# Optimization experiments

Measured on AMD Instinct MI355X. Metric: run time of the kernel, lower is better.

The kernel has to match this reference:

```python
import jax, jax.numpy as jnp
import numpy as np

N = 400000   # active voxels (submanifold: N' == N)
K3 = 27      # kernel_size**3
D = 64       # in_channels
DP = 64      # out_channels


def setup_inputs() -> dict:
    key = jax.random.key(0)
    k1, k2, k3 = jax.random.split(key, 3)
    feats = jax.random.normal(k1, (N, D), dtype=jnp.float32)
    # neighbor index table: indices[k, n] = row of feats contributing at kernel
    # offset k for output site n; negative would mean 'no neighbor' (masked).
    indices = jax.random.randint(k2, (K3, N), 0, N, dtype=jnp.int64)
    weight = jax.random.normal(k3, (K3, D, DP), dtype=jnp.float32)
    return {"feats": feats, "indices": indices, "weight": weight}


def reference(feats, indices, weight):
    # Submanifold sparse conv as implicit GEMM:
    #   out[n] = sum_k feats[indices[k, n]] @ weight[k]   (skip indices < 0)
    # Scan over the K^3 kernel offsets (fixed, small) to avoid materializing
    # the full [K3, N, D] gathered tensor.
    n_out = indices.shape[1]
    dp = weight.shape[2]

    def body(acc, kw):
        idx, w = kw                                   # idx: [N'], w: [D, DP]
        valid = (idx >= 0)[:, None]                   # [N', 1]
        g = jnp.where(valid, feats[jnp.maximum(idx, 0)], 0.0)  # [N', D]
        return acc + g @ w, None

    init = jnp.zeros((n_out, dp), dtype=feats.dtype)
    out, _ = jax.lax.scan(body, init, (indices, weight))
    return out
```

## Files before the change

kernel.cpp:

```cpp
#include <hip/hip_runtime.h>
#include <hip/hip_bf16.h>
#include <stdint.h>

typedef __bf16 bf16_t;
typedef bf16_t bf16x8 __attribute__((ext_vector_type(8)));
typedef float f32x4 __attribute__((ext_vector_type(4)));

#define D_IN 64
#define D_OUT 64
#define BM 256
#define NTHREADS 512

#define GLOAD_LDS16(gsrc, ldst)                                                     \
    __builtin_amdgcn_global_load_lds(                                               \
        (const __attribute__((address_space(1))) uint32_t*)(gsrc),                  \
        (__attribute__((address_space(3))) uint32_t*)(ldst), 16, 0, 0)

__device__ __forceinline__ uint32_t swz(int row, int col) {
    return (uint32_t)((row * 128 + col * 2) ^ ((row & 7) << 4));
}

__global__ void convert_feats(const float* __restrict__ feats,
                              bf16_t* __restrict__ fb,
                              int n_elems, int total8) {
    int g = blockIdx.x * blockDim.x + threadIdx.x;
    for (; g < total8; g += gridDim.x * blockDim.x) {
        const int e = g * 8;
        bf16x8 v = {};
        if (e < n_elems) {
            f32x4 a = *(const f32x4*)(feats + e);
            f32x4 b = *(const f32x4*)(feats + e + 4);
            #pragma unroll
            for (int i = 0; i < 4; ++i) {
                v[i]     = (bf16_t)a[i];
                v[i + 4] = (bf16_t)b[i];
            }
        }
        *(bf16x8*)(fb + e) = v;
    }
}

__global__ void convert_weight(const float* __restrict__ w,
                               bf16_t* __restrict__ wtb, int k3) {
    const int k = blockIdx.x;
    const int tid = threadIdx.x;
    const int dp = tid >> 3;
    const int cp = tid & 7;
    const int d0 = (cp ^ (dp & 7)) * 8;
    const float* src = w + (size_t)k * (D_IN * D_OUT) + (size_t)d0 * D_OUT + dp;
    bf16x8 v;
    #pragma unroll
    for (int j = 0; j < 8; ++j) v[j] = (bf16_t)src[j * D_OUT];
    *(bf16x8*)((char*)wtb + (size_t)k * 8192 + tid * 16) = v;
}

__global__ __launch_bounds__(NTHREADS, 4) void subm_conv_256(
    const bf16_t* __restrict__ fb,
    const int* __restrict__ indices,
    const bf16_t* __restrict__ wtb,
    float* __restrict__ out,
    int n_vox, int k3)
{
    __shared__ __align__(16) bf16_t As[2][BM * 64];
    __shared__ __align__(16) bf16_t Bs[2][64 * 64];

    const int tid  = threadIdx.x;
    const int lane = tid & 63;
    const int wv   = tid >> 6;
    const int l15  = lane & 15;
    const int l4   = lane >> 4;
    const int wr   = (wv >> 1) * 64;
    const int wc   = (wv & 1) * 32;
    const int n0   = blockIdx.x * BM;

    const int rbase = wv * 32 + (lane >> 3);
    const uint32_t so = (uint32_t)(((lane & 7) ^ ((lane >> 3) & 7)) * 16);

    int ia0, ia1, ia2, ia3;

    #define LOADIDX(kk) do {                                                   \
        const int* ip = indices + (size_t)(kk) * n_vox + n0 + rbase;           \
        ia0 = (n0 + rbase      < n_vox) ? ip[0]  : -1;                         \
        ia1 = (n0 + rbase + 8  < n_vox) ? ip[8]  : -1;                         \
        ia2 = (n0 + rbase + 16 < n_vox) ? ip[16] : -1;                         \
        ia3 = (n0 + rbase + 24 < n_vox) ? ip[24] : -1;                         \
    } while (0)

    #define STAGE(buf, kk) do {                                                \
        GLOAD_LDS16((const char*)wtb + (size_t)(kk) * 8192 + tid * 16,         \
                    (char*)&Bs[buf][0] + wv * 1024);                           \
        const size_t r0_ = (size_t)((ia0 >= 0 && ia0 < n_vox) ? ia0 : n_vox);  \
        const size_t r1_ = (size_t)((ia1 >= 0 && ia1 < n_vox) ? ia1 : n_vox);  \
        const size_t r2_ = (size_t)((ia2 >= 0 && ia2 < n_vox) ? ia2 : n_vox);  \
        const size_t r3_ = (size_t)((ia3 >= 0 && ia3 < n_vox) ? ia3 : n_vox);  \
        char* ad_ = (char*)&As[buf][0] + wv * 4096;                            \
        GLOAD_LDS16((const char*)fb + r0_ * 128 + so, ad_);                    \
        GLOAD_LDS16((const char*)fb + r1_ * 128 + so, ad_ + 1024);             \
        GLOAD_LDS16((const char*)fb + r2_ * 128 + so, ad_ + 2048);             \
        GLOAD_LDS16((const char*)fb + r3_ * 128 + so, ad_ + 3072);             \
    } while (0)

    f32x4 acc[4][2];
    #pragma unroll
    for (int i = 0; i < 4; ++i)
        #pragma unroll
        for (int j = 0; j < 2; ++j)
            acc[i][j] = (f32x4){0.f, 0.f, 0.f, 0.f};

    LOADIDX(0);
    STAGE(0, 0);
    if (k3 > 1) LOADIDX(1);

    for (int k = 0; k < k3; ++k) {
        __syncthreads();

        if (k + 1 < k3) STAGE((k + 1) & 1, k + 1);
        if (k + 2 < k3) LOADIDX(k + 2);

        const char* ab = (const char*)&As[k & 1][0];
        const char* bb = (const char*)&Bs[k & 1][0];
        #pragma unroll
        for (int ks = 0; ks < 2; ++ks) {
            const int kc = ks * 32 + l4 * 8;
            bf16x8 b0 = *(const bf16x8*)(bb + swz(wc + l15,      kc));
            bf16x8 b1 = *(const bf16x8*)(bb + swz(wc + 16 + l15, kc));
            #pragma unroll
            for (int mi = 0; mi < 4; ++mi) {
                bf16x8 a = *(const bf16x8*)(ab + swz(wr + mi * 16 + l15, kc));
                acc[mi][0] = __builtin_amdgcn_mfma_f32_16x16x32_bf16(a, b0, acc[mi][0], 0, 0, 0);
                acc[mi][1] = __builtin_amdgcn_mfma_f32_16x16x32_bf16(a, b1, acc[mi][1], 0, 0, 0);
            }
        }
    }

    #pragma unroll
    for (int mi = 0; mi < 4; ++mi)
        #pragma unroll
        for (int ni = 0; ni < 2; ++ni)
            #pragma unroll
            for (int j = 0; j < 4; ++j) {
                const int row = n0 + wr + mi * 16 + l4 * 4 + j;
                const int col = wc + ni * 16 + l15;
                if (row < n_vox)
                    out[(size_t)row * D_OUT + col] = acc[mi][ni][j];
            }
    #undef LOADIDX
    #undef STAGE
}

__global__ __launch_bounds__(512, 1) void subm_conv_mfma_v1(
    const float* __restrict__ feats,
    const int* __restrict__ indices,
    const float* __restrict__ weight,
    float* __restrict__ out,
    int n_vox, int k3)
{
    __shared__ bf16_t As[128 * 64];
    __shared__ bf16_t Bs[64 * 64];

    const int tid  = threadIdx.x;
    const int lane = tid & 63;
    const int wv   = tid >> 6;
    const int wr   = (wv >> 1) * 32;
    const int wc   = (wv & 1) * 32;
    const int l15  = lane & 15;
    const int l4   = lane >> 4;
    const int n0   = blockIdx.x * 128;

    const int ar = tid >> 2;
    const int ac = (tid & 3) * 16;
    const int bdp = tid & 63;
    const int bd0 = (tid >> 6) * 8;

    f32x4 acc[2][2];
    #pragma unroll
    for (int i = 0; i < 2; ++i)
        #pragma unroll
        for (int j = 0; j < 2; ++j)
            acc[i][j] = (f32x4){0.f, 0.f, 0.f, 0.f};

    for (int k = 0; k < k3; ++k) {
        __syncthreads();
        {
            const int n = n0 + ar;
            int idx = (n < n_vox) ? indices[(size_t)k * n_vox + n] : -1;
            bf16x8 v0 = {}, v1 = {};
            if (idx >= 0) {
                const float* src = feats + (size_t)idx * D_IN + ac;
                f32x4 f0 = *(const f32x4*)(src + 0);
                f32x4 f1 = *(const f32x4*)(src + 4);
                f32x4 f2 = *(const f32x4*)(src + 8);
                f32x4 f3 = *(const f32x4*)(src + 12);
                #pragma unroll
                for (int i = 0; i < 4; ++i) {
                    v0[i]     = (bf16_t)f0[i];
                    v0[i + 4] = (bf16_t)f1[i];
                    v1[i]     = (bf16_t)f2[i];
                    v1[i + 4] = (bf16_t)f3[i];
                }
            }
            *(bf16x8*)((char*)As + swz(ar, ac))     = v0;
            *(bf16x8*)((char*)As + swz(ar, ac + 8)) = v1;
        }
        {
            const float* wsrc = weight + (size_t)k * (D_IN * D_OUT) + (size_t)bd0 * D_OUT + bdp;
            bf16x8 v;
            #pragma unroll
            for (int i = 0; i < 8; ++i) v[i] = (bf16_t)wsrc[i * D_OUT];
            *(bf16x8*)((char*)Bs + swz(bdp, bd0)) = v;
        }
        __syncthreads();
        #pragma unroll
        for (int ks = 0; ks < 2; ++ks) {
            const int kc = ks * 32 + l4 * 8;
            bf16x8 a0 = *(const bf16x8*)((char*)As + swz(wr + l15,      kc));
            bf16x8 a1 = *(const bf16x8*)((char*)As + swz(wr + 16 + l15, kc));
            bf16x8 b0 = *(const bf16x8*)((char*)Bs + swz(wc + l15,      kc));
            bf16x8 b1 = *(const bf16x8*)((char*)Bs + swz(wc + 16 + l15, kc));
            acc[0][0] = __builtin_amdgcn_mfma_f32_16x16x32_bf16(a0, b0, acc[0][0], 0, 0, 0);
            acc[0][1] = __builtin_amdgcn_mfma_f32_16x16x32_bf16(a0, b1, acc[0][1], 0, 0, 0);
            acc[1][0] = __builtin_amdgcn_mfma_f32_16x16x32_bf16(a1, b0, acc[1][0], 0, 0, 0);
            acc[1][1] = __builtin_amdgcn_mfma_f32_16x16x32_bf16(a1, b1, acc[1][1], 0, 0, 0);
        }
    }

    #pragma unroll
    for (int mi = 0; mi < 2; ++mi)
        #pragma unroll
        for (int ni = 0; ni < 2; ++ni)
            #pragma unroll
            for (int j = 0; j < 4; ++j) {
                const int row = n0 + wr + mi * 16 + l4 * 4 + j;
                const int col = wc + ni * 16 + l15;
                if (row < n_vox)
                    out[(size_t)row * D_OUT + col] = acc[mi][ni][j];
            }
}

extern "C" void kernel_launch(void* const* d_in, const int* in_sizes, int n_in,
                              void* d_out, int out_size, void* d_ws, size_t ws_size,
                              hipStream_t stream) {
    const float* feats   = (const float*)d_in[0];
    const int*   indices = (const int*)d_in[1];
    const float* weight  = (const float*)d_in[2];
    float* out = (float*)d_out;

    const int n_vox = in_sizes[0] / D_IN;
    const int k3    = in_sizes[2] / (D_IN * D_OUT);

    const size_t fb_bytes  = (size_t)(n_vox + 1) * D_IN * sizeof(bf16_t);
    const size_t wt_off    = (fb_bytes + 255) & ~(size_t)255;
    const size_t wt_bytes  = (size_t)k3 * 64 * 64 * sizeof(bf16_t);
    const size_t need      = wt_off + wt_bytes;

    if (ws_size >= need && k3 >= 2) {
        bf16_t* fb  = (bf16_t*)((char*)d_ws);
        bf16_t* wtb = (bf16_t*)((char*)d_ws + wt_off);

        const int n_elems = n_vox * D_IN;
        const int total8  = (n_vox + 1) * (D_IN / 8);
        int cblocks = (total8 + 255) / 256;
        if (cblocks > 2048) cblocks = 2048;
        convert_feats<<<cblocks, 256, 0, stream>>>(feats, fb, n_elems, total8);
        convert_weight<<<k3, 512, 0, stream>>>(weight, wtb, k3);

        const int grid = (n_vox + BM - 1) / BM;
        subm_conv_256<<<grid, NTHREADS, 0, stream>>>(fb, indices, wtb, out, n_vox, k3);
    } else {
        const int grid = (n_vox + 127) / 128;
        subm_conv_mfma_v1<<<grid, 512, 0, stream>>>(feats, indices, weight, out, n_vox, k3);
    }
}
```

Before: 257.5 us.

## Load weights from global into registers, shrink tile to 192 rows for occupancy

```diff
diff --git a/kernel.cpp b/kernel.cpp
--- a/kernel.cpp
+++ b/kernel.cpp
@@ -8,7 +8,7 @@
 
 #define D_IN 64
 #define D_OUT 64
-#define BM 256
+#define BM 192
 #define NTHREADS 512
 
 #define GLOAD_LDS16(gsrc, ldst)                                                     \
@@ -41,111 +41,119 @@
 }
 
 __global__ void convert_weight(const float* __restrict__ w,
-                               bf16_t* __restrict__ wtb, int k3) {
+                               bf16_t* __restrict__ wt, int k3) {
     const int k = blockIdx.x;
     const int tid = threadIdx.x;
     const int dp = tid >> 3;
-    const int cp = tid & 7;
-    const int d0 = (cp ^ (dp & 7)) * 8;
+    const int d0 = (tid & 7) * 8;
     const float* src = w + (size_t)k * (D_IN * D_OUT) + (size_t)d0 * D_OUT + dp;
     bf16x8 v;
     #pragma unroll
     for (int j = 0; j < 8; ++j) v[j] = (bf16_t)src[j * D_OUT];
-    *(bf16x8*)((char*)wtb + (size_t)k * 8192 + tid * 16) = v;
-}
-
-__global__ __launch_bounds__(NTHREADS, 4) void subm_conv_256(
+    *(bf16x8*)((char*)wt + (size_t)k * 8192 + dp * 128 + d0 * 2) = v;
+}
+
+__global__ __launch_bounds__(NTHREADS, 6) void subm_conv_192(
     const bf16_t* __restrict__ fb,
     const int* __restrict__ indices,
-    const bf16_t* __restrict__ wtb,
+    const bf16_t* __restrict__ wt,
     float* __restrict__ out,
     int n_vox, int k3)
 {
     __shared__ __align__(16) bf16_t As[2][BM * 64];
-    __shared__ __align__(16) bf16_t Bs[2][64 * 64];
 
     const int tid  = threadIdx.x;
     const int lane = tid & 63;
     const int wv   = tid >> 6;
     const int l15  = lane & 15;
     const int l4   = lane >> 4;
-    const int wr   = (wv >> 1) * 64;
-    const int wc   = (wv & 1) * 32;
+    const int wr   = (wv & 1) * 96;
+    const int wc   = (wv >> 1) * 16;
     const int n0   = blockIdx.x * BM;
 
-    const int rbase = wv * 32 + (lane >> 3);
+    const int rbase = wv * 24 + (lane >> 3);
     const uint32_t so = (uint32_t)(((lane & 7) ^ ((lane >> 3) & 7)) * 16);
 
-    int ia0, ia1, ia2, ia3;
+    int ia0, ia1, ia2;
 
     #define LOADIDX(kk) do {                                                   \
         const int* ip = indices + (size_t)(kk) * n_vox + n0 + rbase;           \
         ia0 = (n0 + rbase      < n_vox) ? ip[0]  : -1;                         \
         ia1 = (n0 + rbase + 8  < n_vox) ? ip[8]  : -1;                         \
         ia2 = (n0 + rbase + 16 < n_vox) ? ip[16] : -1;                         \
-        ia3 = (n0 + rbase + 24 < n_vox) ? ip[24] : -1;                         \
     } while (0)
 
     #define STAGE(buf, kk) do {                                                \
-        GLOAD_LDS16((const char*)wtb + (size_t)(kk) * 8192 + tid * 16,         \
-                    (char*)&Bs[buf][0] + wv * 1024);                           \
         const size_t r0_ = (size_t)((ia0 >= 0 && ia0 < n_vox) ? ia0 : n_vox);  \
         const size_t r1_ = (size_t)((ia1 >= 0 && ia1 < n_vox) ? ia1 : n_vox);  \
         const size_t r2_ = (size_t)((ia2 >= 0 && ia2 < n_vox) ? ia2 : n_vox);  \
-        const size_t r3_ = (size_t)((ia3 >= 0 && ia3 < n_vox) ? ia3 : n_vox);  \
-        char* ad_ = (char*)&As[buf][0] + wv * 4096;                            \
+        char* ad_ = (char*)&As[buf][0] + wv * 3072;                            \
         GLOAD_LDS16((const char*)fb + r0_ * 128 + so, ad_);                    \
         GLOAD_LDS16((const char*)fb + r1_ * 128 + so, ad_ + 1024);             \
         GLOAD_LDS16((const char*)fb + r2_ * 128 + so, ad_ + 2048);             \
-        GLOAD_LDS16((const char*)fb + r3_ * 128 + so, ad_ + 3072);             \
-    } while (0)
-
-    f32x4 acc[4][2];
-    #pragma unroll
-    for (int i = 0; i < 4; ++i)
-        #pragma unroll
-        for (int j = 0; j < 2; ++j)
-            acc[i][j] = (f32x4){0.f, 0.f, 0.f, 0.f};
+    } while (0)
+
+    #define LOADB(b0_, b1_, kk) do {                                           \
+        const char* wb_ = (const char*)wt + (size_t)(kk) * 8192                \
+                        + (size_t)(wc + l15) * 128 + l4 * 16;                  \
+        b0_ = *(const bf16x8*)(wb_);                                           \
+        b1_ = *(const bf16x8*)(wb_ + 64);                                      \
+    } while (0)
+
+    #define MFMA_BODY(buf, b0_, b1_) do {                                      \
+        const char* ab_ = (const char*)&As[buf][0];                            \
+        _Pragma("unroll")                                                      \
+        for (int mi = 0; mi < 6; ++mi) {                                       \
+            bf16x8 a0_ = *(const bf16x8*)(ab_ + swz(wr + mi * 16 + l15, l4 * 8));       \
+            acc[mi] = __builtin_amdgcn_mfma_f32_16x16x32_bf16(a0_, b0_, acc[mi], 0, 0, 0); \
+        }                                                                      \
+        _Pragma("unroll")                                                      \
+        for (int mi = 0; mi < 6; ++mi) {                                       \
+            bf16x8 a1_ = *(const bf16x8*)(ab_ + swz(wr + mi * 16 + l15, 32 + l4 * 8));  \
+            acc[mi] = __builtin_amdgcn_mfma_f32_16x16x32_bf16(a1_, b1_, acc[mi], 0, 0, 0); \
+        }                                                                      \
+    } while (0)
+
+    f32x4 acc[6];
+    #pragma unroll
+    for (int i = 0; i < 6; ++i)
+        acc[i] = (f32x4){0.f, 0.f, 0.f, 0.f};
+
+    bf16x8 bE0, bE1, bO0, bO1;
 
     LOADIDX(0);
     STAGE(0, 0);
+    LOADB(bE0, bE1, 0);
     if (k3 > 1) LOADIDX(1);
 
-    for (int k = 0; k < k3; ++k) {
-        __syncthreads();
-
-        if (k + 1 < k3) STAGE((k + 1) & 1, k + 1);
+    int k = 0;
+    while (true) {
+        __syncthreads();
+        if (k + 1 < k3) { STAGE(1, k + 1); LOADB(bO0, bO1, k + 1); }
         if (k + 2 < k3) LOADIDX(k + 2);
-
-        const char* ab = (const char*)&As[k & 1][0];
-        const char* bb = (const char*)&Bs[k & 1][0];
-        #pragma unroll
-        for (int ks = 0; ks < 2; ++ks) {
-            const int kc = ks * 32 + l4 * 8;
-            bf16x8 b0 = *(const bf16x8*)(bb + swz(wc + l15,      kc));
-            bf16x8 b1 = *(const bf16x8*)(bb + swz(wc + 16 + l15, kc));
-            #pragma unroll
-            for (int mi = 0; mi < 4; ++mi) {
-                bf16x8 a = *(const bf16x8*)(ab + swz(wr + mi * 16 + l15, kc));
-                acc[mi][0] = __builtin_amdgcn_mfma_f32_16x16x32_bf16(a, b0, acc[mi][0], 0, 0, 0);
-                acc[mi][1] = __builtin_amdgcn_mfma_f32_16x16x32_bf16(a, b1, acc[mi][1], 0, 0, 0);
-            }
-        }
-    }
-
-    #pragma unroll
-    for (int mi = 0; mi < 4; ++mi)
-        #pragma unroll
-        for (int ni = 0; ni < 2; ++ni)
-            #pragma unroll
-            for (int j = 0; j < 4; ++j) {
-                const int row = n0 + wr + mi * 16 + l4 * 4 + j;
-                const int col = wc + ni * 16 + l15;
-                if (row < n_vox)
-                    out[(size_t)row * D_OUT + col] = acc[mi][ni][j];
-            }
+        MFMA_BODY(0, bE0, bE1);
+        ++k; if (k >= k3) break;
+
+        __syncthreads();
+        if (k + 1 < k3) { STAGE(0, k + 1); LOADB(bE0, bE1, k + 1); }
+        if (k + 2 < k3) LOADIDX(k + 2);
+        MFMA_BODY(1, bO0, bO1);
+        ++k; if (k >= k3) break;
+    }
+
+    #pragma unroll
+    for (int mi = 0; mi < 6; ++mi)
+        #pragma unroll
+        for (int j = 0; j < 4; ++j) {
+            const int row = n0 + wr + mi * 16 + l4 * 4 + j;
+            const int col = wc + l15;
+            if (row < n_vox)
+                out[(size_t)row * D_OUT + col] = acc[mi][j];
+        }
     #undef LOADIDX
     #undef STAGE
+    #undef LOADB
+    #undef MFMA_BODY
 }
 
 __global__ __launch_bounds__(512, 1) void subm_conv_mfma_v1(
@@ -199,6 +207,9 @@
                     v1[i + 4] = (bf16_t)f3[i];
                 }
             }
+            auto swz = [](int row, int col) -> uint32_t {
+                return (uint32_t)((row * 128 + col * 2) ^ ((row & 7) << 4));
+            };
             *(bf16x8*)((char*)As + swz(ar, ac))     = v0;
             *(bf16x8*)((char*)As + swz(ar, ac + 8)) = v1;
         }
@@ -207,6 +218,9 @@
             bf16x8 v;
             #pragma unroll
             for (int i = 0; i < 8; ++i) v[i] = (bf16_t)wsrc[i * D_OUT];
+            auto swz = [](int row, int col) -> uint32_t {
+                return (uint32_t)((row * 128 + col * 2) ^ ((row & 7) << 4));
+            };
             *(bf16x8*)((char*)Bs + swz(bdp, bd0)) = v;
         }
         __syncthreads();
@@ -254,18 +268,18 @@
     const size_t need      = wt_off + wt_bytes;
 
     if (ws_size >= need && k3 >= 2) {
-        bf16_t* fb  = (bf16_t*)((char*)d_ws);
-        bf16_t* wtb = (bf16_t*)((char*)d_ws + wt_off);
+        bf16_t* fb = (bf16_t*)((char*)d_ws);
+        bf16_t* wt = (bf16_t*)((char*)d_ws + wt_off);
 
         const int n_elems = n_vox * D_IN;
         const int total8  = (n_vox + 1) * (D_IN / 8);
         int cblocks = (total8 + 255) / 256;
         if (cblocks > 2048) cblocks = 2048;
         convert_feats<<<cblocks, 256, 0, stream>>>(feats, fb, n_elems, total8);
-        convert_weight<<<k3, 512, 0, stream>>>(weight, wtb, k3);
+        convert_weight<<<k3, 512, 0, stream>>>(weight, wt, k3);
 
         const int grid = (n_vox + BM - 1) / BM;
-        subm_conv_256<<<grid, NTHREADS, 0, stream>>>(fb, indices, wtb, out, n_vox, k3);
+        subm_conv_192<<<grid, NTHREADS, 0, stream>>>(fb, indices, wt, out, n_vox, k3);
     } else {
         const int grid = (n_vox + 127) / 128;
         subm_conv_mfma_v1<<<grid, 512, 0, stream>>>(feats, indices, weight, out, n_vox, k3);
```

After: 249.9 us. 2.9% less time.
